# Kernel optimization log

Measured on AMD Instinct MI355X. Metric: run time of the kernel, lower is better.

The kernel has to match this reference:

```python
import jax, jax.numpy as jnp
import numpy as np
import math

DIM = 2048
NUM_HEADS = 32
HEAD_DIM = DIM // NUM_HEADS  # 64; HEAD_DIM//2 == NUM_HEADS (required by original rope broadcasting)
SEQ_LEN = 2048
BATCH = 2
ROPE_BASE = 10000.0


def apply_rope(inputs, positions):
    # Faithful to original: positions is [L]; sinusoid broadcasts to [1, L, H/2, 1]
    # and then multiplies [B, L, N, H/2] -- the original code relies on N == H/2.
    head_dim = inputs.shape[-1]
    fraction = 2.0 * jnp.arange(head_dim // 2, dtype=inputs.dtype) / head_dim
    timescale = ROPE_BASE ** fraction                      # [H/2]
    sinusoid = positions[:, None] / timescale[None, None, :]  # [1, L, H/2]
    sinusoid = sinusoid[..., None]                         # [1, L, H/2, 1]
    sin = jnp.sin(sinusoid)
    cos = jnp.cos(sinusoid)
    first, second = jnp.split(inputs, 2, axis=-1)          # each [B, L, N, H/2]
    return jnp.concatenate([first * cos - second * sin,
                            second * cos + first * sin], axis=-1)


def setup_inputs() -> dict:
    key = jax.random.key(0)
    ks = jax.random.split(key, 9)
    s = 0.02
    inp = {
        'x': jax.random.normal(ks[0], (BATCH, SEQ_LEN, DIM), dtype=jnp.float32),
        'wq_w': jax.random.normal(ks[1], (DIM, DIM), dtype=jnp.float32) * s,
        'wq_b': jnp.zeros((DIM,), dtype=jnp.float32),
        'wk_w': jax.random.normal(ks[2], (DIM, DIM), dtype=jnp.float32) * s,
        'wk_b': jnp.zeros((DIM,), dtype=jnp.float32),
        'wv_w': jax.random.normal(ks[3], (DIM, DIM), dtype=jnp.float32) * s,
        'wv_b': jnp.zeros((DIM,), dtype=jnp.float32),
        'wo_w': jax.random.normal(ks[4], (DIM, DIM), dtype=jnp.float32) * s,
        'wo_b': jnp.zeros((DIM,), dtype=jnp.float32),
    }
    return inp


def reference(x, wq_w, wq_b, wk_w, wk_b, wv_w, wv_b, wo_w, wo_b):
    B, L, _ = x.shape
    N, H = NUM_HEADS, HEAD_DIM
    q = (x @ wq_w.T + wq_b).reshape(B, L, N, H)
    k = (x @ wk_w.T + wk_b).reshape(B, L, N, H)
    v = (x @ wv_w.T + wv_b).reshape(B, L, N, H)
    positions = jnp.arange(L, dtype=x.dtype)
    q = apply_rope(q, positions)
    k = apply_rope(k, positions)
    # [B, N, L, H]
    q = q.transpose(0, 2, 1, 3)
    k = k.transpose(0, 2, 1, 3)
    v = v.transpose(0, 2, 1, 3)
    scale = math.sqrt(H)
    scores = jnp.einsum('bnqh,bnkh->bnqk', q, k) / scale   # [B, N, L, L]
    causal = jnp.tril(jnp.ones((L, L), dtype=bool))
    scores = jnp.where(causal[None, None], scores, -jnp.inf)
    attn = jax.nn.softmax(scores, axis=-1)
    context = jnp.einsum('bnqk,bnkh->bnqh', attn, v)        # [B, N, L, H]
    context = context.transpose(0, 2, 1, 3).reshape(B, L, DIM)
    return context @ wo_w.T + wo_b
```

## Files before the change

kernel.cpp:

```cpp
#include <hip/hip_runtime.h>
#include <stdint.h>

#define D_MODEL 2048
#define SEQLEN  2048

typedef float f32x4  __attribute__((ext_vector_type(4)));
typedef float f32x16 __attribute__((ext_vector_type(16)));
typedef int   i32x4  __attribute__((ext_vector_type(4)));
typedef short s16x4  __attribute__((ext_vector_type(4)));
typedef __bf16 bf16x8 __attribute__((ext_vector_type(8)));

__device__ __forceinline__ unsigned short f2bf(float f) {
  union { float f; uint32_t u; } x; x.f = f;
  uint32_t r = (x.u + 0x7FFFu + ((x.u >> 16) & 1u)) >> 16;
  return (unsigned short)r;
}

__device__ __forceinline__ bf16x8 as_bf16x8(i32x4 v) {
  union { i32x4 i; bf16x8 b; } u; u.i = v; return u.b;
}

#define MFMA16(acc, a, b) \
  acc = __builtin_amdgcn_mfma_f32_16x16x32_bf16(as_bf16x8(a), as_bf16x8(b), acc, 0, 0, 0)
#define MFMA32(acc, a, b) \
  acc = __builtin_amdgcn_mfma_f32_32x32x16_bf16(as_bf16x8(a), as_bf16x8(b), acc, 0, 0, 0)

__device__ __forceinline__ void gload16(const void* g, void* lds) {
  __builtin_amdgcn_global_load_lds(
      (const __attribute__((address_space(1))) unsigned int*)(uintptr_t)g,
      (__attribute__((address_space(3))) unsigned int*)(uint32_t)(uintptr_t)lds,
      16, 0, 0);
}

__global__ void cvt_bf16_k(const float* __restrict__ in,
                           unsigned short* __restrict__ out, int n4) {
  int i = blockIdx.x * 256 + threadIdx.x;
  if (i < n4) {
    f32x4 v = *(const f32x4*)&in[(size_t)i * 4];
    s16x4 o;
#pragma unroll
    for (int j = 0; j < 4; ++j) o[j] = (short)f2bf(v[j]);
    *(s16x4*)&out[(size_t)i * 4] = o;
  }
}

template <int BM, int BN, int NW, int G, int MODE>
__global__ __launch_bounds__(NW * 64) void gemm2p(
    const unsigned short* __restrict__ A,
    const unsigned short* __restrict__ W0,
    const unsigned short* __restrict__ W1,
    const unsigned short* __restrict__ W2,
    const float* __restrict__ bias0,
    const float* __restrict__ bias1,
    const float* __restrict__ bias2,
    unsigned short* __restrict__ O0,
    unsigned short* __restrict__ O1,
    unsigned short* __restrict__ O2,
    float* __restrict__ Of) {
  constexpr int PLANE_E = (BM + BN) * 32;
  __shared__ alignas(16) unsigned short L[4 * PLANE_E];

  const int t = threadIdx.x;
  const int w = t >> 6, l = t & 63;
  const int wm = w >> 1, wn = w & 1;
  const int band = l >> 4, ln = l & 15;

  const int bx = blockIdx.x;
  const int m0 = blockIdx.y * BM;

  const unsigned short* Wm;
  const float* bias;
  int nloc, mat;
  if constexpr (MODE == 0) {
    mat = bx >> 4;
    nloc = (bx & 15) * BN;
    Wm = mat == 0 ? W0 : (mat == 1 ? W1 : W2);
    bias = mat == 0 ? bias0 : (mat == 1 ? bias1 : bias2);
  } else {
    mat = 0;
    nloc = bx * BN;
    Wm = W0;
    bias = bias0;
  }

  auto stage = [&](int p, int ktile, int b) {
    unsigned short* dst = L + (b * 2 + p) * PLANE_E;
    const int kcol = ktile * 64 + p * 32;
#pragma unroll
    for (int i = 0; i < G; ++i) {
      const int idx = w * G + i;
      const int row = idx * 16 + (l >> 2);
      const int gblk = (l & 3) ^ ((row >> 1) & 3);
      const unsigned short* src =
          (idx * 16 < BM) ? &A[(size_t)(m0 + row) * D_MODEL + kcol + gblk * 8]
                          : &Wm[(size_t)(nloc + row - BM) * D_MODEL + kcol + gblk * 8];
      gload16(src, dst + idx * 512);
    }
  };

  f32x4 acc[4][4] = {};

  stage(0, 0, 0);
  stage(1, 0, 0);
  if constexpr (G == 3) asm volatile("s_waitcnt vmcnt(3)" ::: "memory");
  else                  asm volatile("s_waitcnt vmcnt(4)" ::: "memory");
  __builtin_amdgcn_s_barrier();

  for (int kt = 0; kt < 32; ++kt) {
    const int rb = kt & 1;
    const int ktn = (kt + 1) & 31;
#pragma unroll
    for (int p = 0; p < 2; ++p) {
      const unsigned short* Apl = L + (rb * 2 + p) * PLANE_E;
      const unsigned short* Bpl = Apl + BM * 32;
      i32x4 av[4], bv[4];
#pragma unroll
      for (int mf = 0; mf < 4; ++mf) {
        const int row = wm * 64 + mf * 16 + ln;
        av[mf] = *(const i32x4*)&Apl[row * 32 + (((band ^ (row >> 1)) & 3) << 3)];
      }
#pragma unroll
      for (int nf = 0; nf < 4; ++nf) {
        const int row = wn * 64 + nf * 16 + ln;
        bv[nf] = *(const i32x4*)&Bpl[row * 32 + (((band ^ (row >> 1)) & 3) << 3)];
      }
      stage(p, ktn, rb ^ 1);
      __builtin_amdgcn_s_barrier();
      asm volatile("s_waitcnt lgkmcnt(0)" ::: "memory");
      __builtin_amdgcn_sched_barrier(0);
      __builtin_amdgcn_s_setprio(1);
#pragma unroll
      for (int mf = 0; mf < 4; ++mf)
#pragma unroll
        for (int nf = 0; nf < 4; ++nf)
          MFMA16(acc[mf][nf], av[mf], bv[nf]);
      __builtin_amdgcn_s_setprio(0);
      if constexpr (G == 3) asm volatile("s_waitcnt vmcnt(3)" ::: "memory");
      else                  asm volatile("s_waitcnt vmcnt(4)" ::: "memory");
      __builtin_amdgcn_s_barrier();
    }
  }
  asm volatile("s_waitcnt vmcnt(0)" ::: "memory");

  float bb[4];
#pragma unroll
  for (int nf = 0; nf < 4; ++nf) bb[nf] = bias[nloc + wn * 64 + nf * 16 + ln];

  if constexpr (MODE == 0) {
    unsigned short* Out = mat == 0 ? O0 : (mat == 1 ? O1 : O2);
    const bool rope = (mat < 2);
    const int head = (nloc + wn * 64) >> 6;
    const float ts = powf(10000.0f, (float)head * (1.0f / 32.0f));
#pragma unroll
    for (int mf = 0; mf < 4; ++mf) {
#pragma unroll
      for (int r = 0; r < 4; ++r) {
        const int row = m0 + wm * 64 + mf * 16 + band * 4 + r;
        float vals[4];
#pragma unroll
        for (int nf = 0; nf < 4; ++nf) vals[nf] = acc[mf][nf][r] + bb[nf];
        if (rope) {
          const float pos = (float)(row & (SEQLEN - 1));
          float sv, cv;
          sincosf(pos / ts, &sv, &cv);
#pragma unroll
          for (int pp = 0; pp < 2; ++pp) {
            const float f0 = vals[pp], s0 = vals[pp + 2];
            vals[pp]     = f0 * cv - s0 * sv;
            vals[pp + 2] = s0 * cv + f0 * sv;
          }
        }
#pragma unroll
        for (int nf = 0; nf < 4; ++nf)
          Out[(size_t)row * D_MODEL + nloc + wn * 64 + nf * 16 + ln] = f2bf(vals[nf]);
      }
    }
  } else {
#pragma unroll
    for (int mf = 0; mf < 4; ++mf)
#pragma unroll
      for (int r = 0; r < 4; ++r) {
        const int row = m0 + wm * 64 + mf * 16 + band * 4 + r;
#pragma unroll
        for (int nf = 0; nf < 4; ++nf)
          Of[(size_t)row * D_MODEL + nloc + wn * 64 + nf * 16 + ln] =
              acc[mf][nf][r] + bb[nf];
      }
  }
}

__global__ __launch_bounds__(256) void attn_fwd(
    const unsigned short* __restrict__ Q, const unsigned short* __restrict__ K,
    const unsigned short* __restrict__ V, unsigned short* __restrict__ O) {
  __shared__ alignas(16) unsigned short Ks[64 * 64];
  __shared__ alignas(16) unsigned short Vt[64 * 80];

  const int t = threadIdx.x;
  const int w = t >> 6, l = t & 63;
  const int l31 = l & 31, t5 = l >> 5;
  const int bx = blockIdx.x, head = blockIdx.y, b = blockIdx.z;
  const int h0 = head * 64;
  const size_t rb = (size_t)b * SEQLEN;

  const int vg = t & 7, vrow = t >> 3;
  const int kdr = l >> 3, kdb = l & 7;

  for (int pi = 0; pi < 2; ++pi) {
    const int qt = pi ? (15 - bx) : bx;
    const int q0 = qt * 128;
    const int qg = q0 + w * 32 + l31;

    i32x4 qf[4];
#pragma unroll
    for (int hk = 0; hk < 4; ++hk)
      qf[hk] = *(const i32x4*)&Q[(rb + qg) * D_MODEL + h0 + hk * 16 + t5 * 8];

    f32x16 oacc[2] = {};
    float lsum = 0.f;

    const int nkt = qt * 2 + 2;
    for (int kt = 0; kt < nkt; ++kt) {
      const int k0 = kt * 64;
#pragma unroll
      for (int i = 0; i < 2; ++i) {
        const int drow = (i * 4 + w) * 8 + kdr;
        const int sblk = kdb ^ (drow & 7);
        gload16(&K[(rb + k0 + drow) * D_MODEL + h0 + sblk * 8], &Ks[(i * 4 + w) * 512]);
      }
#pragma unroll
      for (int i = 0; i < 2; ++i) {
        const int r = i * 32 + vrow, c8 = vg * 8;
        i32x4 vv = *(const i32x4*)&V[(rb + k0 + r) * D_MODEL + h0 + c8];
        union { i32x4 v; unsigned short s[8]; } u; u.v = vv;
#pragma unroll
        for (int j = 0; j < 8; ++j) Vt[(c8 + j) * 80 + (r ^ c8)] = u.s[j];
      }
      __syncthreads();

      f32x16 sacc[2] = {};
#pragma unroll
      for (int kvf = 0; kvf < 2; ++kvf) {
        const int krow = kvf * 32 + l31;
#pragma unroll
        for (int hk = 0; hk < 4; ++hk) {
          i32x4 a = *(const i32x4*)&Ks[krow * 64 + ((2 * hk + t5) ^ (krow & 7)) * 8];
          MFMA32(sacc[kvf], a, qf[hk]);
        }
      }

      const bool needmask = (k0 + 64 > q0 + w * 32);
      uint32_t W[2][4][2];
#pragma unroll
      for (int kvf = 0; kvf < 2; ++kvf)
#pragma unroll
        for (int g = 0; g < 4; ++g)
#pragma unroll
          for (int p = 0; p < 2; ++p) {
            uint32_t wd = 0;
#pragma unroll
            for (int e = 0; e < 2; ++e) {
              const int reg = 4 * g + 2 * p + e;
              const int kvl = kvf * 32 + 8 * g + 4 * t5 + 2 * p + e;
              float pv = __expf(sacc[kvf][reg] * 0.125f);
              if (needmask && (k0 + kvl > qg)) pv = 0.f;
              lsum += pv;
              wd |= (uint32_t)f2bf(pv) << (16 * e);
            }
            W[kvf][g][p] = wd;
          }

#pragma unroll
      for (int ks = 0; ks < 4; ++ks) {
        const int kvf = ks >> 1;
        const int gA = 2 * (ks & 1), gB = gA + 1;
        const uint32_t O0 = t5 ? W[kvf][gB][0] : W[kvf][gA][0];
        const uint32_t O1 = t5 ? W[kvf][gB][1] : W[kvf][gA][1];
        const uint32_t E0 = t5 ? W[kvf][gA][0] : W[kvf][gB][0];
        const uint32_t E1 = t5 ? W[kvf][gA][1] : W[kvf][gB][1];
        const uint32_t X0 = (uint32_t)__shfl_xor((int)E0, 32);
        const uint32_t X1 = (uint32_t)__shfl_xor((int)E1, 32);
        i32x4 pf;
        pf[0] = (int)(t5 ? X0 : O0);
        pf[1] = (int)(t5 ? X1 : O1);
        pf[2] = (int)(t5 ? O0 : X0);
        pf[3] = (int)(t5 ? O1 : X1);
#pragma unroll
        for (int hf = 0; hf < 2; ++hf) {
          const int h = hf * 32 + l31;
          i32x4 vb = *(const i32x4*)&Vt[h * 80 + ((ks * 16 + t5 * 8) ^ ((h >> 3) * 8))];
          MFMA32(oacc[hf], pf, vb);
        }
      }
      __syncthreads();
    }

    lsum += __shfl_xor(lsum, 32);
    const float inv = 1.0f / lsum;

#pragma unroll
    for (int g2 = 0; g2 < 4; ++g2)
#pragma unroll
      for (int rr = 0; rr < 4; ++rr) {
        const int rowl = rr + 8 * g2 + 4 * t5;
        const float invr = __shfl(inv, (l & 32) + rowl);
        const size_t gr = rb + q0 + w * 32 + rowl;
#pragma unroll
        for (int hf = 0; hf < 2; ++hf)
          O[gr * D_MODEL + h0 + hf * 32 + l31] = f2bf(oacc[hf][4 * g2 + rr] * invr);
      }
  }
}

extern "C" void kernel_launch(void* const* d_in, const int* in_sizes, int n_in,
                              void* d_out, int out_size, void* d_ws, size_t ws_size,
                              hipStream_t stream) {
  const float* x    = (const float*)d_in[0];
  const float* wq_w = (const float*)d_in[1];
  const float* wq_b = (const float*)d_in[2];
  const float* wk_w = (const float*)d_in[3];
  const float* wk_b = (const float*)d_in[4];
  const float* wv_w = (const float*)d_in[5];
  const float* wv_b = (const float*)d_in[6];
  const float* wo_w = (const float*)d_in[7];
  const float* wo_b = (const float*)d_in[8];
  float* out = (float*)d_out;

  unsigned short* ws  = (unsigned short*)d_ws;
  unsigned short* xb  = ws;
  unsigned short* wqb = xb  + 8388608;
  unsigned short* wkb = wqb + 4194304;
  unsigned short* wvb = wkb + 4194304;
  unsigned short* wob = wvb + 4194304;
  unsigned short* qb  = wob + 4194304;
  unsigned short* kb  = qb  + 8388608;
  unsigned short* vb  = kb  + 8388608;
  unsigned short* cb  = xb;

  cvt_bf16_k<<<8192, 256, 0, stream>>>(x, xb, 2097152);
  cvt_bf16_k<<<4096, 256, 0, stream>>>(wq_w, wqb, 1048576);
  cvt_bf16_k<<<4096, 256, 0, stream>>>(wk_w, wkb, 1048576);
  cvt_bf16_k<<<4096, 256, 0, stream>>>(wv_w, wvb, 1048576);
  cvt_bf16_k<<<4096, 256, 0, stream>>>(wo_w, wob, 1048576);

  gemm2p<256, 128, 8, 3, 0><<<dim3(48, 16), 512, 0, stream>>>(
      xb, wqb, wkb, wvb, wq_b, wk_b, wv_b, qb, kb, vb, nullptr);

  attn_fwd<<<dim3(8, 32, 2), 256, 0, stream>>>(qb, kb, vb, cb);

  gemm2p<128, 128, 4, 4, 1><<<dim3(16, 32), 256, 0, stream>>>(
      cb, wob, nullptr, nullptr, wo_b, nullptr, nullptr,
      nullptr, nullptr, nullptr, out);
}
```

Measured before the change: 283.8 us.

## Double-buffer K/V tiles in attention and retile QKV projection GEMM

The attention kernel now keeps two LDS buffers for K and transposed V. It prefetches the next tile's K (async global-to-LDS) and V (into registers) while running MFMAs on the current tile, then writes the transposed V after the compute, so there is one barrier per iteration instead of two. LDS use per block roughly doubles, which may reduce occupancy. Separately, the QKV projection GEMM switches from 256x128 tiles with 512 threads to 128x128 tiles with 256 threads, doubling the grid.

```diff
diff --git a/kernel.cpp b/kernel.cpp
--- a/kernel.cpp
+++ b/kernel.cpp
@@ -192,8 +192,8 @@
 __global__ __launch_bounds__(256) void attn_fwd(
     const unsigned short* __restrict__ Q, const unsigned short* __restrict__ K,
     const unsigned short* __restrict__ V, unsigned short* __restrict__ O) {
-  __shared__ alignas(16) unsigned short Ks[64 * 64];
-  __shared__ alignas(16) unsigned short Vt[64 * 80];
+  __shared__ alignas(16) unsigned short Ks[2][64 * 64];
+  __shared__ alignas(16) unsigned short Vt[2][64 * 80];
 
   const int t = threadIdx.x;
   const int w = t >> 6, l = t & 63;
@@ -217,25 +217,49 @@
 
     f32x16 oacc[2] = {};
     float lsum = 0.f;
-
     const int nkt = qt * 2 + 2;
-    for (int kt = 0; kt < nkt; ++kt) {
-      const int k0 = kt * 64;
+
+    {
 #pragma unroll
       for (int i = 0; i < 2; ++i) {
         const int drow = (i * 4 + w) * 8 + kdr;
         const int sblk = kdb ^ (drow & 7);
-        gload16(&K[(rb + k0 + drow) * D_MODEL + h0 + sblk * 8], &Ks[(i * 4 + w) * 512]);
-      }
+        gload16(&K[(rb + drow) * D_MODEL + h0 + sblk * 8], &Ks[0][(i * 4 + w) * 512]);
+      }
+      i32x4 vv[2];
+#pragma unroll
+      for (int i = 0; i < 2; ++i)
+        vv[i] = *(const i32x4*)&V[(rb + i * 32 + vrow) * D_MODEL + h0 + vg * 8];
+      asm volatile("s_waitcnt vmcnt(0)" ::: "memory");
 #pragma unroll
       for (int i = 0; i < 2; ++i) {
         const int r = i * 32 + vrow, c8 = vg * 8;
-        i32x4 vv = *(const i32x4*)&V[(rb + k0 + r) * D_MODEL + h0 + c8];
-        union { i32x4 v; unsigned short s[8]; } u; u.v = vv;
-#pragma unroll
-        for (int j = 0; j < 8; ++j) Vt[(c8 + j) * 80 + (r ^ c8)] = u.s[j];
-      }
-      __syncthreads();
+        union { i32x4 v; unsigned short s[8]; } u; u.v = vv[i];
+#pragma unroll
+        for (int j = 0; j < 8; ++j) Vt[0][(c8 + j) * 80 + (r ^ c8)] = u.s[j];
+      }
+    }
+    __syncthreads();
+
+    for (int kt = 0; kt < nkt; ++kt) {
+      const int cur = kt & 1, nxt = cur ^ 1;
+      const int k0 = kt * 64;
+      const bool more = (kt + 1 < nkt);
+
+      i32x4 vv[2];
+      if (more) {
+        const int k1 = k0 + 64;
+#pragma unroll
+        for (int i = 0; i < 2; ++i) {
+          const int drow = (i * 4 + w) * 8 + kdr;
+          const int sblk = kdb ^ (drow & 7);
+          gload16(&K[(rb + k1 + drow) * D_MODEL + h0 + sblk * 8],
+                  &Ks[nxt][(i * 4 + w) * 512]);
+        }
+#pragma unroll
+        for (int i = 0; i < 2; ++i)
+          vv[i] = *(const i32x4*)&V[(rb + k1 + i * 32 + vrow) * D_MODEL + h0 + vg * 8];
+      }
 
       f32x16 sacc[2] = {};
 #pragma unroll
@@ -243,7 +267,7 @@
         const int krow = kvf * 32 + l31;
 #pragma unroll
         for (int hk = 0; hk < 4; ++hk) {
-          i32x4 a = *(const i32x4*)&Ks[krow * 64 + ((2 * hk + t5) ^ (krow & 7)) * 8];
+          i32x4 a = *(const i32x4*)&Ks[cur][krow * 64 + ((2 * hk + t5) ^ (krow & 7)) * 8];
           MFMA32(sacc[kvf], a, qf[hk]);
         }
       }
@@ -287,8 +311,19 @@
 #pragma unroll
         for (int hf = 0; hf < 2; ++hf) {
           const int h = hf * 32 + l31;
-          i32x4 vb = *(const i32x4*)&Vt[h * 80 + ((ks * 16 + t5 * 8) ^ ((h >> 3) * 8))];
+          i32x4 vb = *(const i32x4*)&Vt[cur][h * 80 + ((ks * 16 + t5 * 8) ^ ((h >> 3) * 8))];
           MFMA32(oacc[hf], pf, vb);
+        }
+      }
+
+      if (more) {
+        asm volatile("s_waitcnt vmcnt(0)" ::: "memory");
+#pragma unroll
+        for (int i = 0; i < 2; ++i) {
+          const int r = i * 32 + vrow, c8 = vg * 8;
+          union { i32x4 v; unsigned short s[8]; } u; u.v = vv[i];
+#pragma unroll
+          for (int j = 0; j < 8; ++j) Vt[nxt][(c8 + j) * 80 + (r ^ c8)] = u.s[j];
         }
       }
       __syncthreads();
@@ -342,7 +377,7 @@
   cvt_bf16_k<<<4096, 256, 0, stream>>>(wv_w, wvb, 1048576);
   cvt_bf16_k<<<4096, 256, 0, stream>>>(wo_w, wob, 1048576);
 
-  gemm2p<256, 128, 8, 3, 0><<<dim3(48, 16), 512, 0, stream>>>(
+  gemm2p<128, 128, 4, 4, 0><<<dim3(48, 32), 256, 0, stream>>>(
       xb, wqb, wkb, wvb, wq_b, wk_b, wv_b, qb, kb, vb, nullptr);
 
   attn_fwd<<<dim3(8, 32, 2), 256, 0, stream>>>(qb, kb, vb, cb);
```

Measured after the change: 284.2 us. About the same (+0.1%).
